# Optimization experiments

Hardware: AMD Instinct MI355X
Metric: run time of the kernel (lower is better)

Reference implementation:

```python
import jax, jax.numpy as jnp
import numpy as np

BOUND = 1.0
N_RAYS = 2048
TOT = 128        # num_steps (samples per pixel)
IND_S = 16       # indicator_steps
MAX_DEPTHS = 2
HID = 64
EPS = 1e-8


def setup_inputs() -> dict:
    key = jax.random.key(0)
    ks = jax.random.split(key, 13)
    M = N_RAYS * TOT
    rays_o = 0.3 * jax.random.normal(ks[0], (N_RAYS, 3), jnp.float32)
    rd = jax.random.normal(ks[1], (N_RAYS, 3), jnp.float32)
    rays_d = rd / (jnp.linalg.norm(rd, axis=-1, keepdims=True) + EPS)
    env_map = 0.1 * jax.random.normal(ks[2], (3, 128, 256), jnp.float32)
    Wd1 = jax.random.normal(ks[3], (3, HID), jnp.float32) / np.sqrt(3.0)
    Wd2 = jax.random.normal(ks[4], (HID, 3), jnp.float32) / np.sqrt(HID)
    Wf1 = jax.random.normal(ks[5], (6, HID), jnp.float32) / np.sqrt(6.0)
    Ws = jax.random.normal(ks[6], (HID, 3), jnp.float32) / np.sqrt(HID)
    Wdir = jax.random.normal(ks[7], (HID, 3), jnp.float32) / np.sqrt(HID)
    Wrho = jax.random.normal(ks[8], (HID, 3), jnp.float32) / np.sqrt(HID)
    jitter = jax.random.uniform(ks[9], (MAX_DEPTHS, M, IND_S), jnp.float32)
    u_t = jax.random.uniform(ks[10], (MAX_DEPTHS, M), jnp.float32)
    u_scatter = jax.random.uniform(ks[11], (MAX_DEPTHS, M), jnp.float32)
    channel = jax.random.randint(ks[12], (MAX_DEPTHS, M), 0, 3)
    return dict(rays_o=rays_o, rays_d=rays_d, env_map=env_map, Wd1=Wd1, Wd2=Wd2,
                Wf1=Wf1, Ws=Ws, Wdir=Wdir, Wrho=Wrho,
                jitter=jitter, u_t=u_t, u_scatter=u_scatter, channel=channel)


def _density(pts, Wd1, Wd2):
    # stand-in NeRF density field: 3 spectral channels, positive
    return jax.nn.softplus(jnp.sin(pts @ Wd1) @ Wd2)


def _material(o, d, Wf1, Ws, Wdir, Wrho):
    f = jnp.tanh(jnp.concatenate([o, d], axis=-1) @ Wf1)
    sigma_t = jax.nn.softplus(f @ Ws)                     # [M,3]
    dn = f @ Wdir
    d_out = dn / (jnp.linalg.norm(dn, axis=-1, keepdims=True) + EPS)
    fused_rho = jax.nn.sigmoid(f @ Wrho)                  # [M,3]
    return sigma_t, d_out, fused_rho


def _sample_env(env_map, p):
    # equirectangular lookup == torch grid_sample(bilinear, align_corners=False, zero pad)
    x, y, z = p[:, 0], p[:, 1], p[:, 2]
    theta = jnp.nan_to_num(jnp.arctan2(x, -z)) / jnp.pi            # grid x in [-1,1]
    phi = 2.0 / jnp.pi * jnp.nan_to_num(jnp.arccos(y)) - 1.0       # grid y in [-1,1]
    C, H, W = env_map.shape
    ix = ((theta + 1.0) * W - 1.0) * 0.5
    iy = ((phi + 1.0) * H - 1.0) * 0.5
    x0 = jnp.floor(ix); y0 = jnp.floor(iy)
    wx = ix - x0; wy = iy - y0

    def tap(xc, yc, w):
        inb = (xc >= 0) & (xc < W) & (yc >= 0) & (yc < H)
        xi = jnp.clip(xc, 0, W - 1).astype(jnp.int32)
        yi = jnp.clip(yc, 0, H - 1).astype(jnp.int32)
        return (w * inb)[:, None] * env_map[:, yi, xi].T   # [M,3]

    v = (tap(x0, y0, (1 - wx) * (1 - wy)) + tap(x0 + 1, y0, wx * (1 - wy)) +
         tap(x0, y0 + 1, (1 - wx) * wy) + tap(x0 + 1, y0 + 1, wx * wy))
    return jnp.exp(v)


def _render(rays_o, rays_d, env_map, Wd1, Wd2, Wf1, Ws, Wdir, Wrho,
            jitter, u_t, u_scatter, channel):
    M = N_RAYS * TOT
    o = jnp.repeat(rays_o, TOT, axis=0)   # [M,3]
    d = jnp.repeat(rays_d, TOT, axis=0)
    alive = jnp.ones((M,), bool)          # masked version of boolean compaction
    thr = jnp.ones((M, 3), jnp.float32)
    rgbs = jnp.zeros((M, 3), jnp.float32)
    lin = jnp.linspace(0.0, 1.0, IND_S)

    for dep in range(MAX_DEPTHS):
        # ray-sphere intersection (radius=bound)
        a = jnp.sum(d * d, -1)
        b = 2.0 * jnp.sum(d * o, -1)
        c = jnp.sum(o * o, -1) - BOUND ** 2
        delta = b * b - 4.0 * a * c
        alive = alive & (delta > 0.0)
        sq = jnp.sqrt(jnp.maximum(delta, 0.0))
        nears = jnp.maximum((-b - sq) / (2.0 * a), 0.001)
        fars = jnp.maximum((-b + sq) / (2.0 * a), 0.001)
        span = fars - nears

        # stratified indicator samples -> per-channel majorant
        z = nears[:, None] + span[:, None] * lin[None, :]
        z = z + (jitter[dep] - 0.5) * (span[:, None] / IND_S)
        pts = o[:, None, :] + d[:, None, :] * z[:, :, None]          # [M,S,3]
        sigma = _density(pts.reshape(-1, 3), Wd1, Wd2).reshape(M, IND_S, 3)
        ch = channel[dep]
        maj_multi = jnp.maximum(sigma.max(axis=1), 0.001)            # [M,3]
        sig_ch = jnp.take_along_axis(sigma, ch[:, None, None], axis=2)[..., 0]
        maj = jnp.maximum(sig_ch.max(axis=1), 0.001)                 # [M]

        # free-flight sampling (last depth forces hit at far boundary)
        if dep < MAX_DEPTHS - 1:
            t = -jnp.log1p(-u_t[dep]) / maj + nears
        else:
            t = fars
        hit = alive & (t >= fars)

        # environment hit contribution
        denom = jnp.exp(-maj_multi * span[:, None]) / (maj_multi.max(-1, keepdims=True) + EPS) + EPS
        Le = _sample_env(env_map, o + d * fars[:, None])
        contrib = thr * (denom / jax.lax.stop_gradient(denom.mean(-1, keepdims=True))) * Le
        rgbs = rgbs + jnp.where(hit[:, None], contrib, 0.0)
        alive = alive & ~hit
        if dep == MAX_DEPTHS - 1:
            break

        # throughput update + null/real scattering (delta tracking)
        trans = jnp.exp(-maj_multi * (t - nears)[:, None]) / maj_multi.max(-1, keepdims=True)
        den2 = jax.lax.stop_gradient((maj_multi * trans).mean(-1, keepdims=True))
        thr = jnp.where(alive[:, None], thr * trans / den2, thr)
        o = jnp.where(alive[:, None], jax.lax.stop_gradient(o + d * t[:, None]), o)
        sigma_t, d_out, fused_rho = _material(o, d, Wf1, Ws, Wdir, Wrho)
        sp = jnp.minimum(jnp.take_along_axis(sigma_t, ch[:, None], axis=1)[:, 0] / maj, 1.0)
        sm = alive & (u_scatter[dep] < sp)
        d = jnp.where(sm[:, None], d_out, d)
        thr = jnp.where(sm[:, None], thr / (sp[:, None] + EPS) * fused_rho,
              jnp.where(alive[:, None], thr / (1.0 - sp[:, None] + EPS), thr))

    return rgbs.reshape(N_RAYS, TOT, 3).mean(axis=1)   # [N,3]


def reference(rays_o, rays_d, env_map, Wd1, Wd2, Wf1, Ws, Wdir, Wrho,
              jitter, u_t, u_scatter, channel):
    return _render(rays_o, rays_d, env_map, Wd1, Wd2, Wf1, Ws, Wdir, Wrho,
                   jitter, u_t, u_scatter, channel)
```

## Files before the change

### kernel.cpp

```cpp
#include <hip/hip_runtime.h>
#include <math.h>

#define NRAYS 2048
#define TOT   128
#define INDS  16
#define HID   64
#define EPSF  1e-8f
#define MTOT  (NRAYS*TOT)
#define NTAB  256

typedef float f32x2 __attribute__((ext_vector_type(2)));
typedef float f32x4 __attribute__((ext_vector_type(4)));

__device__ __forceinline__ float softplus_f(float x) {
    return fmaxf(x, 0.0f) + __logf(1.0f + __expf(-fabsf(x)));
}
__device__ __forceinline__ float sigmoid_f(float x) {
    return 1.0f / (1.0f + __expf(-x));
}
__device__ __forceinline__ float tanh_fast(float x) {
    float e2 = __expf(2.0f * x);
    return 1.0f - 2.0f / (e2 + 1.0f);
}
__device__ __forceinline__ f32x2 pkmax(f32x2 a, f32x2 b) {
    f32x2 r; r.x = fmaxf(a.x, b.x); r.y = fmaxf(a.y, b.y); return r;
}
__device__ __forceinline__ f32x2 pkfma(f32x2 a, f32x2 b, f32x2 c) {
    return __builtin_elementwise_fma(a, b, c);
}

#define CK(i) ((float)(i)*(1.0f/15.0f) - 0.03125f)

#define MAKE_Z(jA, jB, kbase, nears, span)                                    \
    float s16 = (span) * (1.0f/16.0f);                                        \
    f32x2 z01, z23, z45, z67;                                                 \
    z01.x = fmaf((jA).x, s16, fmaf(span, CK((kbase)+0), nears));              \
    z01.y = fmaf((jA).y, s16, fmaf(span, CK((kbase)+1), nears));              \
    z23.x = fmaf((jA).z, s16, fmaf(span, CK((kbase)+2), nears));              \
    z23.y = fmaf((jA).w, s16, fmaf(span, CK((kbase)+3), nears));              \
    z45.x = fmaf((jB).x, s16, fmaf(span, CK((kbase)+4), nears));              \
    z45.y = fmaf((jB).y, s16, fmaf(span, CK((kbase)+5), nears));              \
    z67.x = fmaf((jB).z, s16, fmaf(span, CK((kbase)+6), nears));              \
    z67.y = fmaf((jB).w, s16, fmaf(span, CK((kbase)+7), nears));

#define TAB_EVAL(zz, mx0, mx1, mx2)                                           \
    {                                                                         \
        float x = ((zz) - ztab0) * invh;                                      \
        x = fminf(fmaxf(x, 0.0f), (float)(NTAB-1) - 1e-3f);                   \
        int i = (int)x; float w = x - (float)i;                               \
        float ta0 = sT0[i], tb0 = sT0[i+1];                                   \
        float ta1 = sT1[i], tb1 = sT1[i+1];                                   \
        float ta2 = sT2[i], tb2 = sT2[i+1];                                   \
        mx0 = fmaxf(mx0, fmaf(w, tb0 - ta0, ta0));                            \
        mx1 = fmaxf(mx1, fmaf(w, tb1 - ta1, ta1));                            \
        mx2 = fmaxf(mx2, fmaf(w, tb2 - ta2, ta2));                            \
    }

__device__ __forceinline__ void env_logv(
    const float* __restrict__ env_map,
    float px, float py, float pz,
    float& v0, float& v1, float& v2)
{
    float theta = atan2f(px, -pz) * (1.0f/3.14159265358979323846f);
    float acv = (fabsf(py) <= 1.0f) ? acosf(py) : 0.0f;
    float phi = 0.63661977236758134308f * acv - 1.0f;
    float ixf = ((theta + 1.0f)*256.0f - 1.0f)*0.5f;
    float iyf = ((phi   + 1.0f)*128.0f - 1.0f)*0.5f;
    float x0f = floorf(ixf), y0f = floorf(iyf);
    float wx = ixf - x0f, wy = iyf - y0f;
    v0 = 0.f; v1 = 0.f; v2 = 0.f;
    auto tap = [&](float xc, float yc, float w) {
        if (xc >= 0.0f && xc < 256.0f && yc >= 0.0f && yc < 128.0f) {
            int xi = (int)xc, yi = (int)yc;
            const float* e = env_map + yi*256 + xi;
            v0 += w * e[0];
            v1 += w * e[128*256];
            v2 += w * e[2*128*256];
        }
    };
    tap(x0f,      y0f,      (1.0f-wx)*(1.0f-wy));
    tap(x0f+1.0f, y0f,      wx*(1.0f-wy));
    tap(x0f,      y0f+1.0f, (1.0f-wx)*wy);
    tap(x0f+1.0f, y0f+1.0f, wx*wy);
}

__global__ __launch_bounds__(256)
void render_kernel(const float* __restrict__ rays_o,
                   const float* __restrict__ rays_d,
                   const float* __restrict__ env_map,
                   const float* __restrict__ Wd1,
                   const float* __restrict__ Wd2,
                   const float* __restrict__ Wf1,
                   const float* __restrict__ Ws,
                   const float* __restrict__ Wdir,
                   const float* __restrict__ Wrho,
                   const float* __restrict__ jitter,
                   const float* __restrict__ u_t,
                   const float* __restrict__ u_scatter,
                   const int*   __restrict__ channel,
                   float* __restrict__ out)
{
    const int ray  = blockIdx.x;
    const int tid  = threadIdx.x;
    const int s    = tid >> 1;
    const int half = tid & 1;
    const int m    = ray * TOT + s;
    const int kbase = half * 8;
    const float INV2PI = 0.15915494309189535f;

    __shared__ float sT0[NTAB];
    __shared__ float sT1[NTAB];
    __shared__ float sT2[NTAB];
    __shared__ f32x4 sP0[TOT];
    __shared__ f32x4 sP1[TOT];
    __shared__ f32x2 sP2[TOT];
    __shared__ float sEnvE[3];
    __shared__ int   sCnt;
    __shared__ float sred[4][3];

    const float4* j0p = (const float4*)(jitter + (size_t)m*INDS + kbase);
    float4 j0A = j0p[0], j0B = j0p[1];
    int   ch = channel[m];
    float ut = u_t[m];
    float us = u_scatter[m];

    float ox = rays_o[ray*3+0], oy = rays_o[ray*3+1], oz = rays_o[ray*3+2];
    float dx = rays_d[ray*3+0], dy = rays_d[ray*3+1], dz = rays_d[ray*3+2];

    if (tid == 0) sCnt = 0;

    float a0g = dx*dx + dy*dy + dz*dz;
    float b0g = 2.0f*(dx*ox + dy*oy + dz*oz);
    float c0g = (ox*ox + oy*oy + oz*oz) - 1.0f;
    float delta0 = b0g*b0g - 4.0f*a0g*c0g;
    bool alive = (delta0 > 0.0f);

    float nears = 0.f, fars = 0.f, span = 0.f, ztab0 = 0.f, invh = 0.f;
    if (alive) {
        float sq = sqrtf(delta0);
        nears = fmaxf((-b0g - sq) / (2.0f*a0g), 0.001f);
        fars  = fmaxf((-b0g + sq) / (2.0f*a0g), 0.001f);
        span  = fars - nears;
        ztab0 = fmaf(-span, 0.03125f, nears);
        float width = span * 1.0625f;
        float hstep = width * (1.0f/(NTAB-1));
        invh = (float)(NTAB-1) / width;
        float zp = fmaf((float)tid, hstep, ztab0);
        float f0 = 0.f, f1 = 0.f, f2 = 0.f;
        float sox = ox*INV2PI, soy = oy*INV2PI, soz = oz*INV2PI;
        float sdx = dx*INV2PI, sdy = dy*INV2PI, sdz = dz*INV2PI;
        #pragma unroll 2
        for (int j = 0; j < HID; ++j) {
            float w1x = Wd1[j], w1y = Wd1[HID+j], w1z = Wd1[2*HID+j];
            float A = fmaf(sox, w1x, fmaf(soy, w1y, soz*w1z));
            float B = fmaf(sdx, w1x, fmaf(sdy, w1y, sdz*w1z));
            float hv = __builtin_amdgcn_sinf(fmaf(zp, B, A));
            f0 = fmaf(hv, Wd2[3*j+0], f0);
            f1 = fmaf(hv, Wd2[3*j+1], f1);
            f2 = fmaf(hv, Wd2[3*j+2], f2);
        }
        sT0[tid] = f0; sT1[tid] = f1; sT2[tid] = f2;
        if (tid == 0) {
            float v0,v1,v2;
            env_logv(env_map, fmaf(dx,fars,ox), fmaf(dy,fars,oy), fmaf(dz,fars,oz),
                     v0,v1,v2);
            sEnvE[0] = __expf(v0); sEnvE[1] = __expf(v1); sEnvE[2] = __expf(v2);
        }
    }
    __syncthreads();

    float thr0 = 1.f, thr1 = 1.f, thr2 = 1.f;
    float rgb0 = 0.f, rgb1 = 0.f, rgb2 = 0.f;
    bool  tab_d1 = false;
    float tadv = 0.f;

    if (alive) {
        MAKE_Z(j0A, j0B, kbase, nears, span)
        float mx0 = -1e30f, mx1 = -1e30f, mx2 = -1e30f;
        TAB_EVAL(z01.x, mx0,mx1,mx2) TAB_EVAL(z01.y, mx0,mx1,mx2)
        TAB_EVAL(z23.x, mx0,mx1,mx2) TAB_EVAL(z23.y, mx0,mx1,mx2)
        TAB_EVAL(z45.x, mx0,mx1,mx2) TAB_EVAL(z45.y, mx0,mx1,mx2)
        TAB_EVAL(z67.x, mx0,mx1,mx2) TAB_EVAL(z67.y, mx0,mx1,mx2)
        mx0 = fmaxf(mx0, __shfl_xor(mx0, 1, 64));
        mx1 = fmaxf(mx1, __shfl_xor(mx1, 1, 64));
        mx2 = fmaxf(mx2, __shfl_xor(mx2, 1, 64));

        float maj0 = fmaxf(softplus_f(mx0), 0.001f);
        float maj1 = fmaxf(softplus_f(mx1), 0.001f);
        float maj2 = fmaxf(softplus_f(mx2), 0.001f);
        float mmax = fmaxf(fmaxf(maj0, maj1), maj2);

        float maj = (ch == 0) ? maj0 : ((ch == 1) ? maj1 : maj2);
        float t   = -__logf(1.0f - ut) / maj + nears;

        if (t >= fars) {
            float den0 = __expf(-maj0*span)/(mmax+EPSF) + EPSF;
            float den1 = __expf(-maj1*span)/(mmax+EPSF) + EPSF;
            float den2 = __expf(-maj2*span)/(mmax+EPSF) + EPSF;
            float idm = 3.0f / (den0+den1+den2);
            rgb0 = den0*idm*sEnvE[0];
            rgb1 = den1*idm*sEnvE[1];
            rgb2 = den2*idm*sEnvE[2];
        } else {
            float tn  = t - nears;
            float imm = 1.0f / mmax;
            float tr0 = __expf(-maj0*tn) * imm;
            float tr1 = __expf(-maj1*tn) * imm;
            float tr2 = __expf(-maj2*tn) * imm;
            float i2m = 3.0f / (maj0*tr0 + maj1*tr1 + maj2*tr2);
            thr0 = tr0 * i2m;
            thr1 = tr1 * i2m;
            thr2 = tr2 * i2m;
            ox = fmaf(dx, t, ox); oy = fmaf(dy, t, oy); oz = fmaf(dz, t, oz);

            float st0=0.f, st1=0.f, st2=0.f;
            float dn0=0.f, dn1=0.f, dn2v=0.f;
            float rh0=0.f, rh1=0.f, rh2=0.f;
            #pragma unroll 2
            for (int j = 0; j < HID; ++j) {
                float f0 = Wf1[j],       f1 = Wf1[HID+j],   f2 = Wf1[2*HID+j];
                float f3 = Wf1[3*HID+j], f4 = Wf1[4*HID+j], f5 = Wf1[5*HID+j];
                float pre = fmaf(ox,f0, fmaf(oy,f1, fmaf(oz,f2,
                            fmaf(dx,f3, fmaf(dy,f4, dz*f5)))));
                float f = tanh_fast(pre);
                st0  = fmaf(f, Ws[3*j+0],   st0);
                st1  = fmaf(f, Ws[3*j+1],   st1);
                st2  = fmaf(f, Ws[3*j+2],   st2);
                dn0  = fmaf(f, Wdir[3*j+0], dn0);
                dn1  = fmaf(f, Wdir[3*j+1], dn1);
                dn2v = fmaf(f, Wdir[3*j+2], dn2v);
                rh0  = fmaf(f, Wrho[3*j+0], rh0);
                rh1  = fmaf(f, Wrho[3*j+1], rh1);
                rh2  = fmaf(f, Wrho[3*j+2], rh2);
            }

            float stch = (ch == 0) ? st0 : ((ch == 1) ? st1 : st2);
            float sp = fminf(softplus_f(stch) / maj, 1.0f);
            if (us < sp) {
                float inr = 1.0f / (sqrtf(dn0*dn0 + dn1*dn1 + dn2v*dn2v) + EPSF);
                float ndx = dn0*inr, ndy = dn1*inr, ndz = dn2v*inr;
                float isp = 1.0f/(sp + EPSF);
                float t0 = thr0 * isp * sigmoid_f(rh0);
                float t1 = thr1 * isp * sigmoid_f(rh1);
                float t2 = thr2 * isp * sigmoid_f(rh2);
                if (half == 0) {
                    int sl = atomicAdd(&sCnt, 1);
                    sP0[sl] = (f32x4){ox, oy, oz, ndx};
                    sP1[sl] = (f32x4){ndy, ndz, t0, t1};
                    sP2[sl] = (f32x2){t2, (float)m};
                }
            } else {
                float iv = 1.0f/(1.0f - sp + EPSF);
                thr0 *= iv; thr1 *= iv; thr2 *= iv;
                tab_d1 = true;
                tadv = t;
            }
        }
    }
    __syncthreads();
    int npool = sCnt;

    if (tab_d1) {
        float a1 = dx*dx + dy*dy + dz*dz;
        float b1 = 2.0f*(dx*ox + dy*oy + dz*oz);
        float c1 = (ox*ox + oy*oy + oz*oz) - 1.0f;
        float delta1 = b1*b1 - 4.0f*a1*c1;
        if (delta1 > 0.0f) {
            const float4* j1p = (const float4*)(jitter + ((size_t)MTOT + m)*INDS + kbase);
            float4 j1A = j1p[0], j1B = j1p[1];
            float sq1    = sqrtf(delta1);
            float nears1 = fmaxf((-b1 - sq1) / (2.0f*a1), 0.001f);
            float fars1  = fmaxf((-b1 + sq1) / (2.0f*a1), 0.001f);
            float span1  = fars1 - nears1;
            MAKE_Z(j1A, j1B, kbase, nears1, span1)
            float mx0 = -1e30f, mx1 = -1e30f, mx2 = -1e30f;
            TAB_EVAL(tadv + z01.x, mx0,mx1,mx2) TAB_EVAL(tadv + z01.y, mx0,mx1,mx2)
            TAB_EVAL(tadv + z23.x, mx0,mx1,mx2) TAB_EVAL(tadv + z23.y, mx0,mx1,mx2)
            TAB_EVAL(tadv + z45.x, mx0,mx1,mx2) TAB_EVAL(tadv + z45.y, mx0,mx1,mx2)
            TAB_EVAL(tadv + z67.x, mx0,mx1,mx2) TAB_EVAL(tadv + z67.y, mx0,mx1,mx2)
            mx0 = fmaxf(mx0, __shfl_xor(mx0, 1, 64));
            mx1 = fmaxf(mx1, __shfl_xor(mx1, 1, 64));
            mx2 = fmaxf(mx2, __shfl_xor(mx2, 1, 64));

            float maj0 = fmaxf(softplus_f(mx0), 0.001f);
            float maj1 = fmaxf(softplus_f(mx1), 0.001f);
            float maj2 = fmaxf(softplus_f(mx2), 0.001f);
            float mmax = fmaxf(fmaxf(maj0, maj1), maj2);

            float den0 = __expf(-maj0*span1)/(mmax+EPSF) + EPSF;
            float den1 = __expf(-maj1*span1)/(mmax+EPSF) + EPSF;
            float den2 = __expf(-maj2*span1)/(mmax+EPSF) + EPSF;
            float idm = 3.0f / (den0+den1+den2);
            rgb0 += thr0 * den0*idm*sEnvE[0];
            rgb1 += thr1 * den1*idm*sEnvE[1];
            rgb2 += thr2 * den2*idm*sEnvE[2];
        }
    }

    {
        const int qlane = tid & 3;
        const int kq    = qlane * 4;
        const float kqf = (float)kq;
        for (int q = tid >> 2; q < npool; q += 64) {
            f32x4 p0 = sP0[q];
            f32x4 p1 = sP1[q];
            f32x2 p2 = sP2[q];
            float pox = p0.x, poy = p0.y, poz = p0.z;
            float pdx = p0.w, pdy = p1.x, pdz = p1.y;
            float pt0 = p1.z, pt1 = p1.w, pt2 = p2.x;
            int   mm  = (int)p2.y;

            float a1 = pdx*pdx + pdy*pdy + pdz*pdz;
            float b1 = 2.0f*(pdx*pox + pdy*poy + pdz*poz);
            float c1 = (pox*pox + poy*poy + poz*poz) - 1.0f;
            float delta1 = b1*b1 - 4.0f*a1*c1;
            if (delta1 > 0.0f) {
                const float4* jp = (const float4*)(jitter + ((size_t)MTOT + mm)*INDS + kq);
                float4 jq = jp[0];
                float sq1    = sqrtf(delta1);
                float nears1 = fmaxf((-b1 - sq1) / (2.0f*a1), 0.001f);
                float fars1  = fmaxf((-b1 + sq1) / (2.0f*a1), 0.001f);
                float span1  = fars1 - nears1;
                float s16q   = span1 * (1.0f/16.0f);
                f32x2 zA, zB;
                zA.x = fmaf(jq.x, s16q, fmaf(span1, (kqf+0.0f)*(1.0f/15.0f) - 0.03125f, nears1));
                zA.y = fmaf(jq.y, s16q, fmaf(span1, (kqf+1.0f)*(1.0f/15.0f) - 0.03125f, nears1));
                zB.x = fmaf(jq.z, s16q, fmaf(span1, (kqf+2.0f)*(1.0f/15.0f) - 0.03125f, nears1));
                zB.y = fmaf(jq.w, s16q, fmaf(span1, (kqf+3.0f)*(1.0f/15.0f) - 0.03125f, nears1));

                float sox = pox*INV2PI, soy = poy*INV2PI, soz = poz*INV2PI;
                float sdx = pdx*INV2PI, sdy = pdy*INV2PI, sdz = pdz*INV2PI;

                f32x2 a0A = {0.f,0.f}, a0B = {0.f,0.f};
                f32x2 a1A = {0.f,0.f}, a1B = {0.f,0.f};
                f32x2 a2A = {0.f,0.f}, a2B = {0.f,0.f};
                #pragma unroll 2
                for (int j = 0; j < HID; ++j) {
                    float w1x = Wd1[j], w1y = Wd1[HID+j], w1z = Wd1[2*HID+j];
                    float A = fmaf(sox, w1x, fmaf(soy, w1y, soz*w1z));
                    float B = fmaf(sdx, w1x, fmaf(sdy, w1y, sdz*w1z));
                    f32x2 A2 = {A, A}, B2 = {B, B};
                    f32x2 gA = pkfma(zA, B2, A2);
                    f32x2 gB = pkfma(zB, B2, A2);
                    f32x2 hA, hB;
                    hA.x = __builtin_amdgcn_sinf(gA.x); hA.y = __builtin_amdgcn_sinf(gA.y);
                    hB.x = __builtin_amdgcn_sinf(gB.x); hB.y = __builtin_amdgcn_sinf(gB.y);
                    float w20 = Wd2[3*j], w21 = Wd2[3*j+1], w22 = Wd2[3*j+2];
                    f32x2 W0 = {w20, w20}, W1 = {w21, w21}, W2 = {w22, w22};
                    a0A = pkfma(hA, W0, a0A); a0B = pkfma(hB, W0, a0B);
                    a1A = pkfma(hA, W1, a1A); a1B = pkfma(hB, W1, a1B);
                    a2A = pkfma(hA, W2, a2A); a2B = pkfma(hB, W2, a2B);
                }
                f32x2 pm0 = pkmax(a0A, a0B);
                f32x2 pm1 = pkmax(a1A, a1B);
                f32x2 pm2 = pkmax(a2A, a2B);
                float mx0 = fmaxf(pm0.x, pm0.y);
                float mx1 = fmaxf(pm1.x, pm1.y);
                float mx2 = fmaxf(pm2.x, pm2.y);
                mx0 = fmaxf(mx0, __shfl_xor(mx0, 1, 64));
                mx1 = fmaxf(mx1, __shfl_xor(mx1, 1, 64));
                mx2 = fmaxf(mx2, __shfl_xor(mx2, 1, 64));
                mx0 = fmaxf(mx0, __shfl_xor(mx0, 2, 64));
                mx1 = fmaxf(mx1, __shfl_xor(mx1, 2, 64));
                mx2 = fmaxf(mx2, __shfl_xor(mx2, 2, 64));

                float maj0 = fmaxf(softplus_f(mx0), 0.001f);
                float maj1 = fmaxf(softplus_f(mx1), 0.001f);
                float maj2 = fmaxf(softplus_f(mx2), 0.001f);
                float mmax = fmaxf(fmaxf(maj0, maj1), maj2);

                float den0 = __expf(-maj0*span1)/(mmax+EPSF) + EPSF;
                float den1 = __expf(-maj1*span1)/(mmax+EPSF) + EPSF;
                float den2 = __expf(-maj2*span1)/(mmax+EPSF) + EPSF;
                float idm = 3.0f / (den0+den1+den2);
                float v0,v1,v2;
                env_logv(env_map, fmaf(pdx,fars1,pox), fmaf(pdy,fars1,poy),
                         fmaf(pdz,fars1,poz), v0,v1,v2);
                if (qlane < 2) {
                    rgb0 += pt0 * den0*idm*__expf(v0);
                    rgb1 += pt1 * den1*idm*__expf(v1);
                    rgb2 += pt2 * den2*idm*__expf(v2);
                }
            }
        }
    }

    float r0 = rgb0, r1 = rgb1, r2 = rgb2;
    #pragma unroll
    for (int off = 32; off > 0; off >>= 1) {
        r0 += __shfl_down(r0, off, 64);
        r1 += __shfl_down(r1, off, 64);
        r2 += __shfl_down(r2, off, 64);
    }
    int wave = tid >> 6;
    if ((tid & 63) == 0) {
        sred[wave][0] = r0; sred[wave][1] = r1; sred[wave][2] = r2;
    }
    __syncthreads();
    if (tid == 0) {
        out[ray*3+0] = (sred[0][0]+sred[1][0]+sred[2][0]+sred[3][0]) * (1.0f/256.0f);
        out[ray*3+1] = (sred[0][1]+sred[1][1]+sred[2][1]+sred[3][1]) * (1.0f/256.0f);
        out[ray*3+2] = (sred[0][2]+sred[1][2]+sred[2][2]+sred[3][2]) * (1.0f/256.0f);
    }
}

extern "C" void kernel_launch(void* const* d_in, const int* in_sizes, int n_in,
                              void* d_out, int out_size, void* d_ws, size_t ws_size,
                              hipStream_t stream) {
    const float* rays_o    = (const float*)d_in[0];
    const float* rays_d    = (const float*)d_in[1];
    const float* env_map   = (const float*)d_in[2];
    const float* Wd1       = (const float*)d_in[3];
    const float* Wd2       = (const float*)d_in[4];
    const float* Wf1       = (const float*)d_in[5];
    const float* Ws        = (const float*)d_in[6];
    const float* Wdir      = (const float*)d_in[7];
    const float* Wrho      = (const float*)d_in[8];
    const float* jitter    = (const float*)d_in[9];
    const float* u_t       = (const float*)d_in[10];
    const float* u_scatter = (const float*)d_in[11];
    const int*   channel   = (const int*)d_in[12];
    float* out = (float*)d_out;

    render_kernel<<<dim3(NRAYS), dim3(256), 0, stream>>>(
        rays_o, rays_d, env_map, Wd1, Wd2, Wf1, Ws, Wdir, Wrho,
        jitter, u_t, u_scatter, channel, out);
}
```

Before: 185.6 us.

## Precompute per-ray material MLP projections in LDS and split hidden loop across thread pairs

New measurement: 168.1 us. 9.4% less time.

```diff
diff --git a/kernel.cpp b/kernel.cpp
--- a/kernel.cpp
+++ b/kernel.cpp
@@ -7,7 +7,7 @@
 #define HID   64
 #define EPSF  1e-8f
 #define MTOT  (NRAYS*TOT)
-#define NTAB  256
+#define NTAB  128
 
 typedef float f32x2 __attribute__((ext_vector_type(2)));
 typedef float f32x4 __attribute__((ext_vector_type(4)));
@@ -111,6 +111,9 @@
     __shared__ float sT0[NTAB];
     __shared__ float sT1[NTAB];
     __shared__ float sT2[NTAB];
+    __shared__ f32x4 sM0[HID];
+    __shared__ f32x4 sM1[HID];
+    __shared__ f32x4 sM2[HID];
     __shared__ f32x4 sP0[TOT];
     __shared__ f32x4 sP1[TOT];
     __shared__ f32x2 sP2[TOT];
@@ -128,6 +131,15 @@
     float dx = rays_d[ray*3+0], dy = rays_d[ray*3+1], dz = rays_d[ray*3+2];
 
     if (tid == 0) sCnt = 0;
+    if (tid < HID) {
+        float f0 = Wf1[tid],       f1 = Wf1[HID+tid],   f2 = Wf1[2*HID+tid];
+        float f3 = Wf1[3*HID+tid], f4 = Wf1[4*HID+tid], f5 = Wf1[5*HID+tid];
+        float P = ox*f0 + oy*f1 + oz*f2 + dx*f3 + dy*f4 + dz*f5;
+        float Q = dx*f0 + dy*f1 + dz*f2;
+        sM0[tid] = (f32x4){P, Q, Ws[3*tid], Ws[3*tid+1]};
+        sM1[tid] = (f32x4){Ws[3*tid+2], Wdir[3*tid], Wdir[3*tid+1], Wdir[3*tid+2]};
+        sM2[tid] = (f32x4){Wrho[3*tid], Wrho[3*tid+1], Wrho[3*tid+2], 0.0f};
+    }
 
     float a0g = dx*dx + dy*dy + dz*dz;
     float b0g = 2.0f*(dx*ox + dy*oy + dz*oz);
@@ -145,21 +157,23 @@
         float width = span * 1.0625f;
         float hstep = width * (1.0f/(NTAB-1));
         invh = (float)(NTAB-1) / width;
-        float zp = fmaf((float)tid, hstep, ztab0);
-        float f0 = 0.f, f1 = 0.f, f2 = 0.f;
-        float sox = ox*INV2PI, soy = oy*INV2PI, soz = oz*INV2PI;
-        float sdx = dx*INV2PI, sdy = dy*INV2PI, sdz = dz*INV2PI;
-        #pragma unroll 2
-        for (int j = 0; j < HID; ++j) {
-            float w1x = Wd1[j], w1y = Wd1[HID+j], w1z = Wd1[2*HID+j];
-            float A = fmaf(sox, w1x, fmaf(soy, w1y, soz*w1z));
-            float B = fmaf(sdx, w1x, fmaf(sdy, w1y, sdz*w1z));
-            float hv = __builtin_amdgcn_sinf(fmaf(zp, B, A));
-            f0 = fmaf(hv, Wd2[3*j+0], f0);
-            f1 = fmaf(hv, Wd2[3*j+1], f1);
-            f2 = fmaf(hv, Wd2[3*j+2], f2);
-        }
-        sT0[tid] = f0; sT1[tid] = f1; sT2[tid] = f2;
+        if (tid < NTAB) {
+            float zp = fmaf((float)tid, hstep, ztab0);
+            float f0 = 0.f, f1 = 0.f, f2 = 0.f;
+            float sox = ox*INV2PI, soy = oy*INV2PI, soz = oz*INV2PI;
+            float sdx = dx*INV2PI, sdy = dy*INV2PI, sdz = dz*INV2PI;
+            #pragma unroll 2
+            for (int j = 0; j < HID; ++j) {
+                float w1x = Wd1[j], w1y = Wd1[HID+j], w1z = Wd1[2*HID+j];
+                float A = fmaf(sox, w1x, fmaf(soy, w1y, soz*w1z));
+                float B = fmaf(sdx, w1x, fmaf(sdy, w1y, sdz*w1z));
+                float hv = __builtin_amdgcn_sinf(fmaf(zp, B, A));
+                f0 = fmaf(hv, Wd2[3*j+0], f0);
+                f1 = fmaf(hv, Wd2[3*j+1], f1);
+                f2 = fmaf(hv, Wd2[3*j+2], f2);
+            }
+            sT0[tid] = f0; sT1[tid] = f1; sT2[tid] = f2;
+        }
         if (tid == 0) {
             float v0,v1,v2;
             env_logv(env_map, fmaf(dx,fars,ox), fmaf(dy,fars,oy), fmaf(dz,fars,oz),
@@ -216,23 +230,33 @@
             float st0=0.f, st1=0.f, st2=0.f;
             float dn0=0.f, dn1=0.f, dn2v=0.f;
             float rh0=0.f, rh1=0.f, rh2=0.f;
+            const int j0 = half * 32;
             #pragma unroll 2
-            for (int j = 0; j < HID; ++j) {
-                float f0 = Wf1[j],       f1 = Wf1[HID+j],   f2 = Wf1[2*HID+j];
-                float f3 = Wf1[3*HID+j], f4 = Wf1[4*HID+j], f5 = Wf1[5*HID+j];
-                float pre = fmaf(ox,f0, fmaf(oy,f1, fmaf(oz,f2,
-                            fmaf(dx,f3, fmaf(dy,f4, dz*f5)))));
+            for (int j = j0; j < j0 + 32; ++j) {
+                f32x4 q0 = sM0[j];
+                f32x4 q1 = sM1[j];
+                f32x4 q2 = sM2[j];
+                float pre = fmaf(t, q0.y, q0.x);
                 float f = tanh_fast(pre);
-                st0  = fmaf(f, Ws[3*j+0],   st0);
-                st1  = fmaf(f, Ws[3*j+1],   st1);
-                st2  = fmaf(f, Ws[3*j+2],   st2);
-                dn0  = fmaf(f, Wdir[3*j+0], dn0);
-                dn1  = fmaf(f, Wdir[3*j+1], dn1);
-                dn2v = fmaf(f, Wdir[3*j+2], dn2v);
-                rh0  = fmaf(f, Wrho[3*j+0], rh0);
-                rh1  = fmaf(f, Wrho[3*j+1], rh1);
-                rh2  = fmaf(f, Wrho[3*j+2], rh2);
+                st0  = fmaf(f, q0.z, st0);
+                st1  = fmaf(f, q0.w, st1);
+                st2  = fmaf(f, q1.x, st2);
+                dn0  = fmaf(f, q1.y, dn0);
+                dn1  = fmaf(f, q1.z, dn1);
+                dn2v = fmaf(f, q1.w, dn2v);
+                rh0  = fmaf(f, q2.x, rh0);
+                rh1  = fmaf(f, q2.y, rh1);
+                rh2  = fmaf(f, q2.z, rh2);
             }
+            st0  += __shfl_xor(st0, 1, 64);
+            st1  += __shfl_xor(st1, 1, 64);
+            st2  += __shfl_xor(st2, 1, 64);
+            dn0  += __shfl_xor(dn0, 1, 64);
+            dn1  += __shfl_xor(dn1, 1, 64);
+            dn2v += __shfl_xor(dn2v, 1, 64);
+            rh0  += __shfl_xor(rh0, 1, 64);
+            rh1  += __shfl_xor(rh1, 1, 64);
+            rh2  += __shfl_xor(rh2, 1, 64);
 
             float stch = (ch == 0) ? st0 : ((ch == 1) ? st1 : st2);
             float sp = fminf(softplus_f(stch) / maj, 1.0f);
```
